# Optimization experiments

Hardware: AMD Instinct MI355X
Metric: run time of the kernel (lower is better)

## Reference

```python
import jax, jax.numpy as jnp
import numpy as np

N_NODES = 100000
N_EDGES = 1200000
D_IN = 64
D_HID = 64
D_OUT = 10
N_GRAPHS = 128


def setup_inputs() -> dict:
    key = jax.random.key(0)
    ks = jax.random.split(key, 8)
    s_in = 1.0 / np.sqrt(D_IN)
    s_hid = 1.0 / np.sqrt(D_HID)
    return {
        "x": jax.random.normal(ks[0], (N_NODES, D_IN), dtype=jnp.float32),
        "W1": jax.random.normal(ks[1], (D_IN, D_HID), dtype=jnp.float32) * s_in,
        "b1": jnp.zeros((D_HID,), dtype=jnp.float32),
        "W2": jax.random.normal(ks[2], (D_HID, D_HID), dtype=jnp.float32) * s_hid,
        "b2": jnp.zeros((D_HID,), dtype=jnp.float32),
        "Wfc": jax.random.normal(ks[3], (D_HID, D_OUT), dtype=jnp.float32) * s_hid,
        "bfc": jnp.zeros((D_OUT,), dtype=jnp.float32),
        "edge_index": jax.random.randint(ks[4], (2, N_EDGES), 0, N_NODES, dtype=jnp.int64),
        "batch": jnp.sort(jax.random.randint(ks[5], (N_NODES,), 0, N_GRAPHS, dtype=jnp.int64)),
    }


def reference(x, W1, b1, W2, b2, Wfc, bfc, edge_index, batch):
    N = x.shape[0]
    # GCNConv (PyG defaults): add self-loops, symmetric normalization D^-1/2 A D^-1/2
    loops = jnp.arange(N, dtype=edge_index.dtype)
    row = jnp.concatenate([edge_index[0], loops])  # source nodes
    col = jnp.concatenate([edge_index[1], loops])  # destination nodes
    deg = jax.ops.segment_sum(jnp.ones_like(col, dtype=x.dtype), col, num_segments=N)
    dinv = jnp.where(deg > 0, jax.lax.rsqrt(deg), 0.0)
    norm = dinv[row] * dinv[col]  # [E+N]

    def gcn_conv(h, W, b):
        h = h @ W                       # [N, d] linear transform (no bias in lin)
        msg = h[row] * norm[:, None]    # gather + normalize, [E+N, d]
        out = jax.ops.segment_sum(msg, col, num_segments=N)  # scatter-add
        return out + b

    h = jax.nn.relu(gcn_conv(x, W1, b1))
    h = jax.nn.relu(gcn_conv(h, W2, b2))

    # global_mean_pool over batch assignment
    s = jax.ops.segment_sum(h, batch, num_segments=N_GRAPHS)                    # [G, d]
    cnt = jax.ops.segment_sum(jnp.ones((N,), dtype=h.dtype), batch, num_segments=N_GRAPHS)
    pooled = s / jnp.maximum(cnt, 1.0)[:, None]

    return pooled @ Wfc + bfc  # [G, D_OUT]
```

## Files before the change

### kernel.cpp

```cpp
#include <hip/hip_runtime.h>
#include <cstdint>


#define NSORT 256
#define SCAP 768

typedef __attribute__((ext_vector_type(8))) short bf16x8;
typedef __attribute__((ext_vector_type(4))) float f32x4;

static __device__ __forceinline__ unsigned int f2bf_r(float f) {
    unsigned int u = __float_as_uint(f);
    return u + 0x7FFFu + ((u >> 16) & 1u);
}
static __device__ __forceinline__ float bflo(unsigned int v) {
    return __uint_as_float(v << 16);
}
static __device__ __forceinline__ float bfhi(unsigned int v) {
    return __uint_as_float(v & 0xFFFF0000u);
}

__global__ __launch_bounds__(256) void hist_k(const int* __restrict__ ecol,
                                              unsigned int* __restrict__ bhist,
                                              float* __restrict__ pooled_zero, int zn,
                                              int E, int chunk, int nbuck) {
    __shared__ unsigned int lh[256];
    lh[threadIdx.x] = 0u;
    __syncthreads();
    if (blockIdx.x == 0) {
        for (int i = threadIdx.x; i < zn; i += 256) pooled_zero[i] = 0.f;
    }
    const int s = blockIdx.x * chunk;
    const int e = min(s + chunk, E);
    const int n4 = (e - s) >> 2;
    const uint4* ec4 = (const uint4*)(ecol + s);
    for (int i = threadIdx.x; i < n4; i += 256) {
        uint4 v = ec4[i];
        atomicAdd(&lh[v.x >> 9], 1u);
        atomicAdd(&lh[v.y >> 9], 1u);
        atomicAdd(&lh[v.z >> 9], 1u);
        atomicAdd(&lh[v.w >> 9], 1u);
    }
    for (int i = s + (n4 << 2) + threadIdx.x; i < e; i += 256)
        atomicAdd(&lh[((unsigned int)ecol[i]) >> 9], 1u);
    __syncthreads();
    if ((int)threadIdx.x < nbuck)
        bhist[threadIdx.x * NSORT + blockIdx.x] = lh[threadIdx.x];
}

__global__ __launch_bounds__(256) void scatter2_k(const int* __restrict__ erow,
                                                  const int* __restrict__ ecol,
                                                  const unsigned int* __restrict__ bhist,
                                                  unsigned int* __restrict__ bbase_out,
                                                  unsigned int* __restrict__ totals_out,
                                                  unsigned int* __restrict__ packed,
                                                  int E, int chunk, int nbuck) {
    __shared__ unsigned int cur[256];
    __shared__ unsigned int sc[256];
    const int t = threadIdx.x;
    const int blk = blockIdx.x;
    unsigned int total = 0u, mine = 0u;
    if (t < nbuck) {
        const uint4* h4 = (const uint4*)(bhist + t * NSORT);
#pragma unroll 8
        for (int i = 0; i < NSORT / 4; ++i) {
            uint4 v = h4[i];
            const int b0 = i * 4;
            total += v.x + v.y + v.z + v.w;
            mine += (b0 + 0 < blk ? v.x : 0u) + (b0 + 1 < blk ? v.y : 0u) +
                    (b0 + 2 < blk ? v.z : 0u) + (b0 + 3 < blk ? v.w : 0u);
        }
    }
    sc[t] = (t < nbuck) ? total : 0u;
    __syncthreads();
    for (int d = 1; d < 256; d <<= 1) {
        unsigned int u2 = (t >= d) ? sc[t - d] : 0u;
        __syncthreads();
        sc[t] += u2;
        __syncthreads();
    }
    const unsigned int base = sc[t] - ((t < nbuck) ? total : 0u);
    if (t < nbuck) {
        cur[t] = base + mine;
        if (blk == 0) {
            bbase_out[t] = base;
            totals_out[t] = total;
        }
    }
    __syncthreads();
    const int s = blk * chunk;
    const int e = min(s + chunk, E);
    const int n4 = (e - s) >> 2;
    const uint4* ec4 = (const uint4*)(ecol + s);
    const uint4* er4 = (const uint4*)(erow + s);
    for (int i = t; i < n4; i += 256) {
        uint4 d = ec4[i];
        uint4 r = er4[i];
        unsigned int p;
        p = atomicAdd(&cur[d.x >> 9], 1u); packed[p] = (r.x << 9) | (d.x & 511u);
        p = atomicAdd(&cur[d.y >> 9], 1u); packed[p] = (r.y << 9) | (d.y & 511u);
        p = atomicAdd(&cur[d.z >> 9], 1u); packed[p] = (r.z << 9) | (d.z & 511u);
        p = atomicAdd(&cur[d.w >> 9], 1u); packed[p] = (r.w << 9) | (d.w & 511u);
    }
    for (int i = s + (n4 << 2) + t; i < e; i += 256) {
        unsigned int d = (unsigned int)ecol[i];
        unsigned int p = atomicAdd(&cur[d >> 9], 1u);
        packed[p] = (((unsigned int)erow[i]) << 9) | (d & 511u);
    }
}

__global__ __launch_bounds__(512) void finegemm_k(const unsigned int* __restrict__ packed,
                                                  const unsigned int* __restrict__ bbase,
                                                  const unsigned int* __restrict__ totals,
                                                  uint2* __restrict__ meta,
                                                  float* __restrict__ dinv,
                                                  unsigned int* __restrict__ srcs,
                                                  const float* __restrict__ x,
                                                  const float* __restrict__ W1,
                                                  unsigned short* __restrict__ G16,
                                                  int N) {
    __shared__ unsigned int fh[512];
    __shared__ unsigned int sc[512];
    __shared__ float dld[512];
    const int k = blockIdx.x;
    const int t = threadIdx.x;
    const unsigned int ebase = bbase[k];
    const unsigned int ecnt = totals[k];
    fh[t] = 0u;
    __syncthreads();
    for (unsigned int j = t; j < ecnt; j += 512)
        atomicAdd(&fh[packed[ebase + j] & 511u], 1u);
    __syncthreads();
    unsigned int v = fh[t];
    sc[t] = v;
    __syncthreads();
    for (int d = 1; d < 512; d <<= 1) {
        unsigned int u2 = (t >= d) ? sc[t - d] : 0u;
        __syncthreads();
        sc[t] += u2;
        __syncthreads();
    }
    const unsigned int excl = sc[t] - v;
    const int node = (k << 9) + t;
    const float dv_t = rsqrtf((float)v + 1.0f);
    dld[t] = dv_t;
    if (node < N) {
        meta[node] = make_uint2(ebase + excl, v);
        dinv[node] = dv_t;
    }
    __syncthreads();
    fh[t] = excl;
    __syncthreads();
    for (unsigned int j = t; j < ecnt; j += 512) {
        unsigned int p = packed[ebase + j];
        unsigned int pos = atomicAdd(&fh[p & 511u], 1u);
        srcs[ebase + pos] = (p >> 9) << 7;
    }
    const int lane = t & 63;
    const int wave = t >> 6;
    const int col = lane & 15;
    const int kg = lane >> 4;
    bf16x8 wf[4][2];
#pragma unroll
    for (int tt = 0; tt < 4; ++tt)
#pragma unroll
        for (int s = 0; s < 2; ++s)
#pragma unroll
            for (int e = 0; e < 8; ++e)
                wf[tt][s][e] =
                    (short)(f2bf_r(W1[(s * 32 + kg * 8 + e) * 64 + tt * 16 + col]) >> 16);
    const int rbase = k << 9;
#pragma unroll
    for (int tile = wave; tile < 32; tile += 8) {
        const int r0 = rbase + tile * 16;
        if (r0 >= N) break;
        const int arow = min(r0 + col, N - 1);
        bf16x8 af0, af1;
        const float4* p = (const float4*)(x + (size_t)arow * 64 + kg * 8);
        float4 q0 = p[0], q1 = p[1], q2 = p[8], q3 = p[9];
        af0[0] = (short)(f2bf_r(q0.x) >> 16); af0[1] = (short)(f2bf_r(q0.y) >> 16);
        af0[2] = (short)(f2bf_r(q0.z) >> 16); af0[3] = (short)(f2bf_r(q0.w) >> 16);
        af0[4] = (short)(f2bf_r(q1.x) >> 16); af0[5] = (short)(f2bf_r(q1.y) >> 16);
        af0[6] = (short)(f2bf_r(q1.z) >> 16); af0[7] = (short)(f2bf_r(q1.w) >> 16);
        af1[0] = (short)(f2bf_r(q2.x) >> 16); af1[1] = (short)(f2bf_r(q2.y) >> 16);
        af1[2] = (short)(f2bf_r(q2.z) >> 16); af1[3] = (short)(f2bf_r(q2.w) >> 16);
        af1[4] = (short)(f2bf_r(q3.x) >> 16); af1[5] = (short)(f2bf_r(q3.y) >> 16);
        af1[6] = (short)(f2bf_r(q3.z) >> 16); af1[7] = (short)(f2bf_r(q3.w) >> 16);
        f32x4 zero = {0.0f, 0.0f, 0.0f, 0.0f};
        f32x4 acc0 = zero, acc1 = zero, acc2 = zero, acc3 = zero;
        acc0 = __builtin_amdgcn_mfma_f32_16x16x32_bf16(af0, wf[0][0], acc0, 0, 0, 0);
        acc1 = __builtin_amdgcn_mfma_f32_16x16x32_bf16(af0, wf[1][0], acc1, 0, 0, 0);
        acc2 = __builtin_amdgcn_mfma_f32_16x16x32_bf16(af0, wf[2][0], acc2, 0, 0, 0);
        acc3 = __builtin_amdgcn_mfma_f32_16x16x32_bf16(af0, wf[3][0], acc3, 0, 0, 0);
        acc0 = __builtin_amdgcn_mfma_f32_16x16x32_bf16(af1, wf[0][1], acc0, 0, 0, 0);
        acc1 = __builtin_amdgcn_mfma_f32_16x16x32_bf16(af1, wf[1][1], acc1, 0, 0, 0);
        acc2 = __builtin_amdgcn_mfma_f32_16x16x32_bf16(af1, wf[2][1], acc2, 0, 0, 0);
        acc3 = __builtin_amdgcn_mfma_f32_16x16x32_bf16(af1, wf[3][1], acc3, 0, 0, 0);
#pragma unroll
        for (int reg = 0; reg < 4; ++reg) {
            const int r = r0 + kg * 4 + reg;
            if (r < N) {
                const float dv = dld[r - rbase];
                unsigned short* gp = G16 + (size_t)r * 64 + col;
                gp[0]  = (unsigned short)(f2bf_r(acc0[reg] * dv) >> 16);
                gp[16] = (unsigned short)(f2bf_r(acc1[reg] * dv) >> 16);
                gp[32] = (unsigned short)(f2bf_r(acc2[reg] * dv) >> 16);
                gp[48] = (unsigned short)(f2bf_r(acc3[reg] * dv) >> 16);
            }
        }
    }
}

__global__ __launch_bounds__(256) void agg_gemm_k(const char* __restrict__ Gb,
                                                  const uint2* __restrict__ meta,
                                                  const unsigned int* __restrict__ srcs,
                                                  const float* __restrict__ dinv,
                                                  const float* __restrict__ bias,
                                                  const float* __restrict__ W2,
                                                  unsigned short* __restrict__ G2,
                                                  int N) {
    __shared__ unsigned int slds[SCAP];
    __shared__ unsigned short hlds[32 * 64];
    uint4* hlds4 = (uint4*)hlds;
    hlds4[threadIdx.x] = make_uint4(0u, 0u, 0u, 0u);

    const int nodeBase = blockIdx.x * 32;
    const int nLast = min(nodeBase + 31, N - 1);
    const unsigned int base = meta[nodeBase].x;
    const uint2 lastm = meta[nLast];
    const unsigned int blen = lastm.x + lastm.y - base;
    for (unsigned int i = threadIdx.x; i < blen && i < SCAP; i += 256)
        slds[i] = srcs[base + i];
    __syncthreads();

    const int lane = threadIdx.x & 63;
    const int grp = lane >> 3;
    const int sub = lane & 7;
    const int node = nodeBase + (threadIdx.x >> 6) * 8 + grp;
    if (node < N) {
        const uint2 oc = meta[node];
        const unsigned int orel = oc.x - base;
        const unsigned int c = oc.y;
        const unsigned int suboff = (unsigned int)sub << 4;
#define LDSRC(i) ((i) < SCAP ? slds[i] : srcs[base + (i)])
        float a0 = 0.f, a1 = 0.f, a2 = 0.f, a3 = 0.f;
        float a4 = 0.f, a5 = 0.f, a6 = 0.f, a7 = 0.f;
#define ACCUM(v)                              \
    do {                                      \
        a0 += bflo((v).x); a1 += bfhi((v).x); \
        a2 += bflo((v).y); a3 += bfhi((v).y); \
        a4 += bflo((v).z); a5 += bfhi((v).z); \
        a6 += bflo((v).w); a7 += bfhi((v).w); \
    } while (0)
        unsigned int j = 0;
        for (; j + 4 <= c; j += 4) {
            unsigned int s0 = LDSRC(orel + j);
            unsigned int s1 = LDSRC(orel + j + 1);
            unsigned int s2 = LDSRC(orel + j + 2);
            unsigned int s3 = LDSRC(orel + j + 3);
            uint4 v0 = *(const uint4*)(Gb + (s0 | suboff));
            uint4 v1 = *(const uint4*)(Gb + (s1 | suboff));
            uint4 v2 = *(const uint4*)(Gb + (s2 | suboff));
            uint4 v3 = *(const uint4*)(Gb + (s3 | suboff));
            ACCUM(v0); ACCUM(v1); ACCUM(v2); ACCUM(v3);
        }
        for (; j < c; ++j) {
            unsigned int s0 = LDSRC(orel + j);
            uint4 v = *(const uint4*)(Gb + (s0 | suboff));
            ACCUM(v);
        }
        {
            uint4 g = *(const uint4*)(Gb + (((unsigned int)node << 7) | suboff));
            ACCUM(g);
        }
        const float dv = dinv[node];
        const float4 b0 = ((const float4*)bias)[sub * 2];
        const float4 b1 = ((const float4*)bias)[sub * 2 + 1];
        float o0 = fmaxf(fmaf(a0, dv, b0.x), 0.0f);
        float o1 = fmaxf(fmaf(a1, dv, b0.y), 0.0f);
        float o2 = fmaxf(fmaf(a2, dv, b0.z), 0.0f);
        float o3 = fmaxf(fmaf(a3, dv, b0.w), 0.0f);
        float o4 = fmaxf(fmaf(a4, dv, b1.x), 0.0f);
        float o5 = fmaxf(fmaf(a5, dv, b1.y), 0.0f);
        float o6 = fmaxf(fmaf(a6, dv, b1.z), 0.0f);
        float o7 = fmaxf(fmaf(a7, dv, b1.w), 0.0f);
        uint4 out;
        out.x = (f2bf_r(o0) >> 16) | (f2bf_r(o1) & 0xFFFF0000u);
        out.y = (f2bf_r(o2) >> 16) | (f2bf_r(o3) & 0xFFFF0000u);
        out.z = (f2bf_r(o4) >> 16) | (f2bf_r(o5) & 0xFFFF0000u);
        out.w = (f2bf_r(o6) >> 16) | (f2bf_r(o7) & 0xFFFF0000u);
        const int row = node - nodeBase;
        hlds4[(row << 3) | (sub ^ (row & 7))] = out;
    }
    __syncthreads();

    const int wid = threadIdx.x >> 6;
    const int rowhalf = wid >> 1;
    const int colpair = wid & 1;
    const int col = lane & 15;
    const int kg = lane >> 4;
    bf16x8 wf[2][2];
#pragma unroll
    for (int ct = 0; ct < 2; ++ct)
#pragma unroll
        for (int s = 0; s < 2; ++s)
#pragma unroll
            for (int e = 0; e < 8; ++e)
                wf[ct][s][e] = (short)(f2bf_r(W2[(s * 32 + kg * 8 + e) * 64 +
                                                 colpair * 32 + ct * 16 + col]) >> 16);
    const int arow = rowhalf * 16 + col;
    const int slot0 = kg ^ (arow & 7);
    bf16x8 af0 = *(const bf16x8*)&hlds4[(arow << 3) | slot0];
    bf16x8 af1 = *(const bf16x8*)&hlds4[(arow << 3) | (slot0 ^ 4)];
    f32x4 zero = {0.0f, 0.0f, 0.0f, 0.0f};
    f32x4 acc0 = zero, acc1 = zero;
    acc0 = __builtin_amdgcn_mfma_f32_16x16x32_bf16(af0, wf[0][0], acc0, 0, 0, 0);
    acc1 = __builtin_amdgcn_mfma_f32_16x16x32_bf16(af0, wf[1][0], acc1, 0, 0, 0);
    acc0 = __builtin_amdgcn_mfma_f32_16x16x32_bf16(af1, wf[0][1], acc0, 0, 0, 0);
    acc1 = __builtin_amdgcn_mfma_f32_16x16x32_bf16(af1, wf[1][1], acc1, 0, 0, 0);
#pragma unroll
    for (int reg = 0; reg < 4; ++reg) {
        const int r = nodeBase + rowhalf * 16 + kg * 4 + reg;
        if (r < N) {
            const float dv = dinv[r];
            unsigned short* gp = G2 + (size_t)r * 64 + colpair * 32 + col;
            gp[0]  = (unsigned short)(f2bf_r(acc0[reg] * dv) >> 16);
            gp[16] = (unsigned short)(f2bf_r(acc1[reg] * dv) >> 16);
        }
    }
}

__global__ __launch_bounds__(256) void agg_pool_k(const char* __restrict__ Gb,
                                                  const uint2* __restrict__ meta,
                                                  const unsigned int* __restrict__ srcs,
                                                  const float* __restrict__ dinv,
                                                  const float* __restrict__ bias,
                                                  const int* __restrict__ batch,
                                                  float* __restrict__ pooled, int N) {
    __shared__ unsigned int slds[SCAP];
    __shared__ unsigned int hl[32 * 32];
    __shared__ float red[8 * 64];
    __shared__ int gb[32];
    const int t = threadIdx.x;
    const int nodeBase = blockIdx.x * 32;
    const int nLast = min(nodeBase + 31, N - 1);
    const unsigned int base = meta[nodeBase].x;
    const uint2 lastm = meta[nLast];
    const unsigned int blen = lastm.x + lastm.y - base;
    for (unsigned int i = t; i < blen && i < SCAP; i += 256)
        slds[i] = srcs[base + i];
    if (t < 32) gb[t] = (nodeBase + t < N) ? batch[nodeBase + t] : -1;
    __syncthreads();

    const int lane = t & 63;
    const int grp = lane >> 3;
    const int sub = lane & 7;
    const int node = nodeBase + (t >> 6) * 8 + grp;
    if (node < N) {
        const uint2 oc = meta[node];
        const unsigned int orel = oc.x - base;
        const unsigned int c = oc.y;
        const unsigned int suboff = (unsigned int)sub << 4;
        float a0 = 0.f, a1 = 0.f, a2 = 0.f, a3 = 0.f;
        float a4 = 0.f, a5 = 0.f, a6 = 0.f, a7 = 0.f;
        unsigned int j = 0;
        for (; j + 4 <= c; j += 4) {
            unsigned int s0 = LDSRC(orel + j);
            unsigned int s1 = LDSRC(orel + j + 1);
            unsigned int s2 = LDSRC(orel + j + 2);
            unsigned int s3 = LDSRC(orel + j + 3);
            uint4 v0 = *(const uint4*)(Gb + (s0 | suboff));
            uint4 v1 = *(const uint4*)(Gb + (s1 | suboff));
            uint4 v2 = *(const uint4*)(Gb + (s2 | suboff));
            uint4 v3 = *(const uint4*)(Gb + (s3 | suboff));
            ACCUM(v0); ACCUM(v1); ACCUM(v2); ACCUM(v3);
        }
        for (; j < c; ++j) {
            unsigned int s0 = LDSRC(orel + j);
            uint4 v = *(const uint4*)(Gb + (s0 | suboff));
            ACCUM(v);
        }
        {
            uint4 g = *(const uint4*)(Gb + (((unsigned int)node << 7) | suboff));
            ACCUM(g);
        }
#undef ACCUM
#undef LDSRC
        const float dv = dinv[node];
        const float4 c0 = ((const float4*)bias)[sub * 2];
        const float4 c1 = ((const float4*)bias)[sub * 2 + 1];
        float o0 = fmaxf(fmaf(a0, dv, c0.x), 0.0f);
        float o1 = fmaxf(fmaf(a1, dv, c0.y), 0.0f);
        float o2 = fmaxf(fmaf(a2, dv, c0.z), 0.0f);
        float o3 = fmaxf(fmaf(a3, dv, c0.w), 0.0f);
        float o4 = fmaxf(fmaf(a4, dv, c1.x), 0.0f);
        float o5 = fmaxf(fmaf(a5, dv, c1.y), 0.0f);
        float o6 = fmaxf(fmaf(a6, dv, c1.z), 0.0f);
        float o7 = fmaxf(fmaf(a7, dv, c1.w), 0.0f);
        const int row = node - nodeBase;
        unsigned int* hp = &hl[row * 32 + sub * 4];
        hp[0] = (f2bf_r(o0) >> 16) | (f2bf_r(o1) & 0xFFFF0000u);
        hp[1] = (f2bf_r(o2) >> 16) | (f2bf_r(o3) & 0xFFFF0000u);
        hp[2] = (f2bf_r(o4) >> 16) | (f2bf_r(o5) & 0xFFFF0000u);
        hp[3] = (f2bf_r(o6) >> 16) | (f2bf_r(o7) & 0xFFFF0000u);
    }
    __syncthreads();

    const int g0 = gb[0];
    const int g1 = gb[nLast - nodeBase];
    const int w = t >> 5;
    const int c2 = t & 31;
    for (int g = g0; g <= g1; ++g) {
        float a0 = 0.f, a1 = 0.f;
        for (int r = w; r < 32; r += 8) {
            if (gb[r] == g) {
                unsigned int v = hl[r * 32 + c2];
                a0 += bflo(v);
                a1 += bfhi(v);
            }
        }
        red[w * 64 + 2 * c2] = a0;
        red[w * 64 + 2 * c2 + 1] = a1;
        __syncthreads();
        if (t < 64) {
            float s = 0.f;
#pragma unroll
            for (int i = 0; i < 8; ++i) s += red[i * 64 + t];
            atomicAdd(&pooled[g * 64 + t], s);
        }
        __syncthreads();
    }
}

__global__ __launch_bounds__(64) void fc_k(const float* __restrict__ pooled,
                                           const int* __restrict__ batch,
                                           const float* __restrict__ Wfc,
                                           const float* __restrict__ bfc,
                                           float* __restrict__ out, int N) {
    __shared__ float p[64];
    const int g = blockIdx.x;
    const int t = threadIdx.x;
    int lo = 0, hi = N;
    while (lo < hi) {
        int mid = (lo + hi) >> 1;
        if (batch[mid] < g) lo = mid + 1; else hi = mid;
    }
    const int start = lo;
    hi = N;
    while (lo < hi) {
        int mid = (lo + hi) >> 1;
        if (batch[mid] < g + 1) lo = mid + 1; else hi = mid;
    }
    const float cc = (float)max(lo - start, 1);
    p[t] = pooled[g * 64 + t] / cc;
    __syncthreads();
    if (t < 10) {
        float a = bfc[t];
#pragma unroll
        for (int k = 0; k < 64; ++k) a = fmaf(p[k], Wfc[k * 10 + t], a);
        out[g * 10 + t] = a;
    }
}

extern "C" void kernel_launch(void* const* d_in, const int* in_sizes, int n_in,
                              void* d_out, int out_size, void* d_ws, size_t ws_size,
                              hipStream_t stream) {
    const float* x     = (const float*)d_in[0];
    const float* W1    = (const float*)d_in[1];
    const float* b1    = (const float*)d_in[2];
    const float* W2    = (const float*)d_in[3];
    const float* b2    = (const float*)d_in[4];
    const float* Wfc   = (const float*)d_in[5];
    const float* bfc   = (const float*)d_in[6];
    const int*   eidx  = (const int*)d_in[7];
    const int*   batch = (const int*)d_in[8];

    const int N = in_sizes[0] / 64;
    const int E = in_sizes[7] / 2;
    const int Gn = out_size / 10;
    const int* erow = eidx;
    const int* ecol = eidx + E;

    const int nbuck = (N + 511) >> 9;
    const int chunk = (((E + NSORT - 1) / NSORT) + 3) & ~3;

    char* ws = (char*)d_ws;
    size_t off = 0;
    auto alloc = [&](size_t bytes) -> void* {
        void* p = ws + off;
        off = (off + bytes + 511) & ~(size_t)511;
        return p;
    };
    uint2*        meta   = (uint2*)alloc((size_t)N * 8);
    float*        dinv   = (float*)alloc((size_t)N * 4);
    unsigned int* totals = (unsigned int*)alloc((size_t)nbuck * 4);
    unsigned int* bbase  = (unsigned int*)alloc((size_t)nbuck * 4);
    unsigned int* srcs   = (unsigned int*)alloc((size_t)E * 4);
    unsigned short* G16  = (unsigned short*)alloc((size_t)N * 64 * 2);
    unsigned short* G2   = (unsigned short*)alloc((size_t)N * 64 * 2);
    unsigned int* packed = (unsigned int*)alloc((size_t)E * 4);
    unsigned int* bhist  = (unsigned int*)alloc((size_t)NSORT * 256 * 4);
    float*        pooled = (float*)alloc((size_t)Gn * 64 * 4);

    const int ZN = Gn * 64;

    hist_k<<<NSORT, 256, 0, stream>>>(ecol, bhist, pooled, ZN, E, chunk, nbuck);
    scatter2_k<<<NSORT, 256, 0, stream>>>(erow, ecol, bhist, bbase, totals,
                                          packed, E, chunk, nbuck);
    finegemm_k<<<nbuck, 512, 0, stream>>>(packed, bbase, totals, meta, dinv,
                                          srcs, x, W1, G16, N);

    const int aggB = (N + 31) / 32;
    agg_gemm_k<<<aggB, 256, 0, stream>>>((const char*)G16, meta, srcs, dinv, b1,
                                         W2, G2, N);
    agg_pool_k<<<aggB, 256, 0, stream>>>((const char*)G2, meta, srcs, dinv, b2,
                                         batch, pooled, N);
    fc_k<<<Gn, 64, 0, stream>>>(pooled, batch, Wfc, bfc, (float*)d_out, N);
}
```

Measured before the change: 106.8 us.

## Sort nodes by degree within blocks and fuse final FC into pooling kernel

Both aggregation kernels now rank the 32 nodes of each block by in-degree and assign them to 8-lane groups in sorted order. Nodes with similar edge counts then share a wavefront, which reduces divergence in the gather loops. The separate fc_k launch is removed: the last block of agg_pool_k, detected with an atomic done counter that hist_k zeroes, computes the mean-pool division and the small FC layer. This trades one kernel launch for a serial tail in one block, plus an extra syncthreads and a rank computation per block.

After: 383.4 us. +258.8%, slower.

```diff
diff --git a/kernel.cpp b/kernel.cpp
--- a/kernel.cpp
+++ b/kernel.cpp
@@ -210,6 +210,25 @@
     }
 }
 
+#define RANK32(meta_, nodeBase_, N_, sdeg_, sidx_)                          \
+    do {                                                                    \
+        if (t < 32) {                                                       \
+            unsigned int d_ = (nodeBase_ + t < N_) ? meta_[nodeBase_ + t].y \
+                                                   : 0u;                    \
+            sdeg_[t] = d_;                                                  \
+        }                                                                   \
+        __syncthreads();                                                    \
+        if (t < 32) {                                                       \
+            unsigned int d_ = sdeg_[t];                                     \
+            int r_ = 0;                                                     \
+            _Pragma("unroll") for (int j_ = 0; j_ < 32; ++j_) {             \
+                unsigned int dj_ = sdeg_[j_];                               \
+                r_ += (dj_ < d_) || (dj_ == d_ && j_ < t);                  \
+            }                                                               \
+            sidx_[r_] = (unsigned char)t;                                   \
+        }                                                                   \
+    } while (0)
+
 __global__ __launch_bounds__(256) void agg_gemm_k(const char* __restrict__ Gb,
                                                   const uint2* __restrict__ meta,
                                                   const unsigned int* __restrict__ srcs,
@@ -220,30 +239,33 @@
                                                   int N) {
     __shared__ unsigned int slds[SCAP];
     __shared__ unsigned short hlds[32 * 64];
+    __shared__ unsigned int sdeg[32];
+    __shared__ unsigned char sidx[32];
     uint4* hlds4 = (uint4*)hlds;
-    hlds4[threadIdx.x] = make_uint4(0u, 0u, 0u, 0u);
+    const int t = threadIdx.x;
+    hlds4[t] = make_uint4(0u, 0u, 0u, 0u);
 
     const int nodeBase = blockIdx.x * 32;
     const int nLast = min(nodeBase + 31, N - 1);
     const unsigned int base = meta[nodeBase].x;
     const uint2 lastm = meta[nLast];
     const unsigned int blen = lastm.x + lastm.y - base;
-    for (unsigned int i = threadIdx.x; i < blen && i < SCAP; i += 256)
+    RANK32(meta, nodeBase, N, sdeg, sidx);
+    for (unsigned int i = t; i < blen && i < SCAP; i += 256)
         slds[i] = srcs[base + i];
     __syncthreads();
 
-    const int lane = threadIdx.x & 63;
+    const int lane = t & 63;
     const int grp = lane >> 3;
     const int sub = lane & 7;
-    const int node = nodeBase + (threadIdx.x >> 6) * 8 + grp;
+    const int row = sidx[(t >> 6) * 8 + grp];
+    const int node = nodeBase + row;
     if (node < N) {
         const uint2 oc = meta[node];
         const unsigned int orel = oc.x - base;
         const unsigned int c = oc.y;
         const unsigned int suboff = (unsigned int)sub << 4;
 #define LDSRC(i) ((i) < SCAP ? slds[i] : srcs[base + (i)])
-        float a0 = 0.f, a1 = 0.f, a2 = 0.f, a3 = 0.f;
-        float a4 = 0.f, a5 = 0.f, a6 = 0.f, a7 = 0.f;
 #define ACCUM(v)                              \
     do {                                      \
         a0 += bflo((v).x); a1 += bfhi((v).x); \
@@ -251,6 +273,8 @@
         a4 += bflo((v).z); a5 += bfhi((v).z); \
         a6 += bflo((v).w); a7 += bfhi((v).w); \
     } while (0)
+        float a0 = 0.f, a1 = 0.f, a2 = 0.f, a3 = 0.f;
+        float a4 = 0.f, a5 = 0.f, a6 = 0.f, a7 = 0.f;
         unsigned int j = 0;
         for (; j + 4 <= c; j += 4) {
             unsigned int s0 = LDSRC(orel + j);
@@ -288,12 +312,11 @@
         out.y = (f2bf_r(o2) >> 16) | (f2bf_r(o3) & 0xFFFF0000u);
         out.z = (f2bf_r(o4) >> 16) | (f2bf_r(o5) & 0xFFFF0000u);
         out.w = (f2bf_r(o6) >> 16) | (f2bf_r(o7) & 0xFFFF0000u);
-        const int row = node - nodeBase;
         hlds4[(row << 3) | (sub ^ (row & 7))] = out;
     }
     __syncthreads();
 
-    const int wid = threadIdx.x >> 6;
+    const int wid = t >> 6;
     const int rowhalf = wid >> 1;
     const int colpair = wid & 1;
     const int col = lane & 15;
@@ -327,6 +350,8 @@
             gp[16] = (unsigned short)(f2bf_r(acc1[reg] * dv) >> 16);
         }
     }
+#undef ACCUM
+#undef LDSRC
 }
 
 __global__ __launch_bounds__(256) void agg_pool_k(const char* __restrict__ Gb,
@@ -335,17 +360,26 @@
                                                   const float* __restrict__ dinv,
                                                   const float* __restrict__ bias,
                                                   const int* __restrict__ batch,
-                                                  float* __restrict__ pooled, int N) {
+                                                  float* __restrict__ pooled,
+                                                  const float* __restrict__ Wfc,
+                                                  const float* __restrict__ bfc,
+                                                  float* __restrict__ out,
+                                                  unsigned int* __restrict__ done,
+                                                  int nblk, int Gn, int N) {
     __shared__ unsigned int slds[SCAP];
     __shared__ unsigned int hl[32 * 32];
     __shared__ float red[8 * 64];
     __shared__ int gb[32];
+    __shared__ unsigned int sdeg[32];
+    __shared__ unsigned char sidx[32];
+    __shared__ unsigned int lastFlag;
     const int t = threadIdx.x;
     const int nodeBase = blockIdx.x * 32;
     const int nLast = min(nodeBase + 31, N - 1);
     const unsigned int base = meta[nodeBase].x;
     const uint2 lastm = meta[nLast];
     const unsigned int blen = lastm.x + lastm.y - base;
+    RANK32(meta, nodeBase, N, sdeg, sidx);
     for (unsigned int i = t; i < blen && i < SCAP; i += 256)
         slds[i] = srcs[base + i];
     if (t < 32) gb[t] = (nodeBase + t < N) ? batch[nodeBase + t] : -1;
@@ -354,12 +388,21 @@
     const int lane = t & 63;
     const int grp = lane >> 3;
     const int sub = lane & 7;
-    const int node = nodeBase + (t >> 6) * 8 + grp;
+    const int row = sidx[(t >> 6) * 8 + grp];
+    const int node = nodeBase + row;
     if (node < N) {
         const uint2 oc = meta[node];
         const unsigned int orel = oc.x - base;
         const unsigned int c = oc.y;
         const unsigned int suboff = (unsigned int)sub << 4;
+#define LDSRC(i) ((i) < SCAP ? slds[i] : srcs[base + (i)])
+#define ACCUM(v)                              \
+    do {                                      \
+        a0 += bflo((v).x); a1 += bfhi((v).x); \
+        a2 += bflo((v).y); a3 += bfhi((v).y); \
+        a4 += bflo((v).z); a5 += bfhi((v).z); \
+        a6 += bflo((v).w); a7 += bfhi((v).w); \
+    } while (0)
         float a0 = 0.f, a1 = 0.f, a2 = 0.f, a3 = 0.f;
         float a4 = 0.f, a5 = 0.f, a6 = 0.f, a7 = 0.f;
         unsigned int j = 0;
@@ -396,7 +439,6 @@
         float o5 = fmaxf(fmaf(a5, dv, c1.y), 0.0f);
         float o6 = fmaxf(fmaf(a6, dv, c1.z), 0.0f);
         float o7 = fmaxf(fmaf(a7, dv, c1.w), 0.0f);
-        const int row = node - nodeBase;
         unsigned int* hp = &hl[row * 32 + sub * 4];
         hp[0] = (f2bf_r(o0) >> 16) | (f2bf_r(o1) & 0xFFFF0000u);
         hp[1] = (f2bf_r(o2) >> 16) | (f2bf_r(o3) & 0xFFFF0000u);
@@ -429,35 +471,43 @@
         }
         __syncthreads();
     }
-}
-
-__global__ __launch_bounds__(64) void fc_k(const float* __restrict__ pooled,
-                                           const int* __restrict__ batch,
-                                           const float* __restrict__ Wfc,
-                                           const float* __restrict__ bfc,
-                                           float* __restrict__ out, int N) {
-    __shared__ float p[64];
-    const int g = blockIdx.x;
-    const int t = threadIdx.x;
-    int lo = 0, hi = N;
-    while (lo < hi) {
-        int mid = (lo + hi) >> 1;
-        if (batch[mid] < g) lo = mid + 1; else hi = mid;
-    }
-    const int start = lo;
-    hi = N;
-    while (lo < hi) {
-        int mid = (lo + hi) >> 1;
-        if (batch[mid] < g + 1) lo = mid + 1; else hi = mid;
-    }
-    const float cc = (float)max(lo - start, 1);
-    p[t] = pooled[g * 64 + t] / cc;
-    __syncthreads();
-    if (t < 10) {
-        float a = bfc[t];
-#pragma unroll
-        for (int k = 0; k < 64; ++k) a = fmaf(p[k], Wfc[k * 10 + t], a);
-        out[g * 10 + t] = a;
+
+    __threadfence();
+    __syncthreads();
+    if (t == 0) {
+        unsigned int prev = __hip_atomic_fetch_add(done, 1u, __ATOMIC_ACQ_REL,
+                                                   __HIP_MEMORY_SCOPE_AGENT);
+        lastFlag = (prev == (unsigned int)(nblk - 1)) ? 1u : 0u;
+    }
+    __syncthreads();
+    if (lastFlag) {
+        __threadfence();
+        if (t < Gn) {
+            const int g = t;
+            int lo = 0, hi = N;
+            while (lo < hi) {
+                int mid = (lo + hi) >> 1;
+                if (batch[mid] < g) lo = mid + 1; else hi = mid;
+            }
+            const int start = lo;
+            hi = N;
+            while (lo < hi) {
+                int mid = (lo + hi) >> 1;
+                if (batch[mid] < g + 1) lo = mid + 1; else hi = mid;
+            }
+            const float inv = 1.0f / (float)max(lo - start, 1);
+            float acc[10];
+#pragma unroll
+            for (int j = 0; j < 10; ++j) acc[j] = bfc[j];
+            for (int k = 0; k < 64; ++k) {
+                const float pv = pooled[g * 64 + k] * inv;
+#pragma unroll
+                for (int j = 0; j < 10; ++j)
+                    acc[j] = fmaf(pv, Wfc[k * 10 + j], acc[j]);
+            }
+#pragma unroll
+            for (int j = 0; j < 10; ++j) out[g * 10 + j] = acc[j];
+        }
     }
 }
 
@@ -499,9 +549,10 @@
     unsigned short* G2   = (unsigned short*)alloc((size_t)N * 64 * 2);
     unsigned int* packed = (unsigned int*)alloc((size_t)E * 4);
     unsigned int* bhist  = (unsigned int*)alloc((size_t)NSORT * 256 * 4);
-    float*        pooled = (float*)alloc((size_t)Gn * 64 * 4);
-
-    const int ZN = Gn * 64;
+    float*        pooled = (float*)alloc((size_t)(Gn * 64 + 16) * 4);
+    unsigned int* done   = (unsigned int*)(pooled + Gn * 64);
+
+    const int ZN = Gn * 64 + 1;
 
     hist_k<<<NSORT, 256, 0, stream>>>(ecol, bhist, pooled, ZN, E, chunk, nbuck);
     scatter2_k<<<NSORT, 256, 0, stream>>>(erow, ecol, bhist, bbase, totals,
@@ -513,6 +564,6 @@
     agg_gemm_k<<<aggB, 256, 0, stream>>>((const char*)G16, meta, srcs, dinv, b1,
                                          W2, G2, N);
     agg_pool_k<<<aggB, 256, 0, stream>>>((const char*)G2, meta, srcs, dinv, b2,
-                                         batch, pooled, N);
-    fc_k<<<Gn, 64, 0, stream>>>(pooled, batch, Wfc, bfc, (float*)d_out, N);
-}
+                                         batch, pooled, Wfc, bfc,
+                                         (float*)d_out, done, aggB, Gn, N);
+}
```
